# Optimization experiments

Hardware: AMD Instinct MI355X
Metric: run time of the kernel (lower is better)

The kernel has to match this reference:

```python
import jax, jax.numpy as jnp
import numpy as np

B, N, D, H = 32, 2048, 65, 64  # batch, seq_len, in_dim+out_dim, hid
GAMMA = 0.0001


def setup_inputs() -> dict:
    key = jax.random.key(0)
    kx, kq, kk, kv = jax.random.split(key, 4)
    x = jax.random.normal(kx, (B, N, D), dtype=jnp.float32)
    std_qk = (GAMMA / D) ** 0.5
    Wq = jax.random.normal(kq, (H, D), dtype=jnp.float32) * std_qk
    Wk = jax.random.normal(kk, (H, D), dtype=jnp.float32) * std_qk
    Wv = jax.random.normal(kv, (D, D), dtype=jnp.float32) * GAMMA
    return {"x": x, "Wq": Wq, "Wk": Wk, "Wv": Wv}


def reference(x, Wq, Wk, Wv):
    # Linear projections (torch nn.Linear: x @ W^T)
    Q = jnp.einsum('bnd,hd->bnh', x, Wq)  # [B, N, H]
    K = jnp.einsum('bnd,hd->bnh', x, Wk)  # [B, N, H]
    V = jnp.einsum('bnd,ed->bne', x, Wv)  # [B, N, D]
    # Non-softmax linear attention: (Q K^T) V, as written in the module
    scores = jnp.einsum('bnh,bmh->bnm', Q, K)  # [B, N, N]
    out = jnp.einsum('bnm,bmd->bnd', scores, V)  # [B, N, D]
    return out
```

## Files before the change

### kernel.cpp

```cpp
#include <hip/hip_runtime.h>

#define BB 32
#define NN 2048
#define DD 65
#define HH 64
#define ST 68
#define TILE (DD * ST)
#define CC 32

__device__ __forceinline__ float4 f4add(float4 a, float4 b) {
  return make_float4(a.x + b.x, a.y + b.y, a.z + b.z, a.w + b.w);
}

#define GL2LDS(g, l)                                             \
  __builtin_amdgcn_global_load_lds(                              \
      (const __attribute__((address_space(1))) void*)(g),        \
      (__attribute__((address_space(3))) void*)(l), 16, 0, 0)

__global__ __launch_bounds__(256, 6) void k1_gram(const float* __restrict__ x,
                                                  float* __restrict__ P) {
  __shared__ __align__(16) float Xl[64 * ST];
  const int t = (int)threadIdx.x;
  const int tx = t & 15, ty = t >> 4;
  const int blk = (int)blockIdx.x;
  const int b = blk >> 5, c = blk & 31;
  const float* src = x + ((size_t)b * NN + (size_t)c * 64) * DD;

  {
#pragma unroll
    for (int p = 0; p < 3; p++) {
      float tmp[6];
      const int cnt = (p == 2) ? 5 : 6;
#pragma unroll
      for (int q = 0; q < 6; q++) {
        const int idx = t + 256 * (6 * p + q);
        if (q < cnt && idx < 64 * DD) tmp[q] = src[idx];
      }
#pragma unroll
      for (int q = 0; q < 6; q++) {
        const int idx = t + 256 * (6 * p + q);
        if (q < cnt && idx < 64 * DD) {
          const int r = idx / DD;
          Xl[r * ST + (idx - r * DD)] = tmp[q];
        }
      }
    }
  }
  __syncthreads();

  float g[4][4] = {};
  float g64[4] = {};
  float gcc = 0.f;
  for (int n = 0; n < 64; n++) {
    float rowf[4], colf[4];
    *(float4*)rowf = *(const float4*)&Xl[n * ST + 4 * ty];
    *(float4*)colf = *(const float4*)&Xl[n * ST + 4 * tx];
    const float x64 = Xl[n * ST + 64];
#pragma unroll
    for (int r = 0; r < 4; r++)
#pragma unroll
      for (int cc = 0; cc < 4; cc++)
        g[r][cc] = fmaf(rowf[r], colf[cc], g[r][cc]);
#pragma unroll
    for (int cc = 0; cc < 4; cc++) g64[cc] = fmaf(x64, colf[cc], g64[cc]);
    gcc = fmaf(x64, x64, gcc);
  }
  float* Pp = P + (size_t)blk * TILE;
#pragma unroll
  for (int r = 0; r < 4; r++)
    *(float4*)&Pp[(4 * ty + r) * ST + 4 * tx] = *(float4*)g[r];
  if (ty == 0) {
    *(float4*)&Pp[64 * ST + 4 * tx] = *(float4*)g64;
#pragma unroll
    for (int cc = 0; cc < 4; cc++)
      Pp[(4 * tx + cc) * ST + 64] = g64[cc];
    if (tx == 0) Pp[64 * ST + 64] = gcc;
  }
}

__global__ __launch_bounds__(256) void kred(const float* __restrict__ P,
                                            float* __restrict__ G) {
  const int t = (int)threadIdx.x;
  const int blk = (int)blockIdx.x;
  const int b = blk / 5, s = blk - b * 5;
  const int Q = TILE / 4;
  const int i4 = s * 256 + t;
  if (i4 < Q) {
    const float4* Pb = (const float4*)(P + (size_t)b * CC * TILE);
    float4 acc = make_float4(0.f, 0.f, 0.f, 0.f);
#pragma unroll
    for (int grp = 0; grp < 4; grp++) {
      float4 v[8];
#pragma unroll
      for (int cc = 0; cc < 8; cc++)
        v[cc] = Pb[(size_t)(8 * grp + cc) * Q + i4];
#pragma unroll
      for (int stp = 4; stp >= 1; stp >>= 1)
#pragma unroll
        for (int cc = 0; cc < stp; cc++) v[cc] = f4add(v[cc], v[cc + stp]);
      acc = f4add(acc, v[0]);
    }
    ((float4*)(G + (size_t)b * TILE))[i4] = acc;
  }
}

__global__ __launch_bounds__(256) void k2_chain(
    const float* __restrict__ Wq, const float* __restrict__ Wk,
    const float* __restrict__ Wv, const float* __restrict__ G,
    float* __restrict__ Tm) {
  __shared__ __align__(16) float WqL[HH * ST];
  __shared__ __align__(16) float WkL[HH * ST];
  __shared__ __align__(16) float GL[TILE];
  __shared__ __align__(16) float WvT[TILE];
  __shared__ __align__(16) float Mr[8 * ST];
  __shared__ __align__(16) float Rr[8 * ST];

  const int t = (int)threadIdx.x;
  const int tx = t & 31, ty = t >> 5;
  const int blk = (int)blockIdx.x;
  const int b = blk / 9, rg = blk - b * 9;
  const int i = 8 * rg + ty;
  const bool alive = (i < DD);
  const int ic = alive ? i : 0;

  {
    float tq[17], tk[17];
#pragma unroll
    for (int q = 0; q < 17; q++) {
      const int idx = t + 256 * q;
      if (idx < HH * DD) { tq[q] = Wq[idx]; tk[q] = Wk[idx]; }
    }
#pragma unroll
    for (int q = 0; q < 17; q++) {
      const int idx = t + 256 * q;
      if (idx < HH * DD) {
        const int r = idx / DD, cc = idx - r * DD;
        WqL[r * ST + cc] = tq[q];
        WkL[r * ST + cc] = tk[q];
      }
    }
  }
  {
    const float4* Gb4 = (const float4*)(G + (size_t)b * TILE);
    float4 tG[5];
#pragma unroll
    for (int q = 0; q < 5; q++) {
      const int i4 = t + 256 * q;
      if (i4 < TILE / 4) tG[q] = Gb4[i4];
    }
#pragma unroll
    for (int q = 0; q < 5; q++) {
      const int i4 = t + 256 * q;
      if (i4 < TILE / 4) *((float4*)GL + i4) = tG[q];
    }
  }
  {
    float tv[17];
#pragma unroll
    for (int q = 0; q < 17; q++) {
      const int idx = t + 256 * q;
      if (idx < DD * DD) tv[q] = Wv[idx];
    }
#pragma unroll
    for (int q = 0; q < 17; q++) {
      const int idx = t + 256 * q;
      if (idx < DD * DD) {
        const int j = idx / DD, k = idx - j * DD;
        WvT[k * ST + j] = tv[q];
      }
    }
  }
  __syncthreads();

  {
    float m0 = 0.f, m1 = 0.f, m2 = 0.f;
    for (int h = 0; h < HH; h++) {
      const float wq = WqL[h * ST + ic];
      m0 = fmaf(wq, WkL[h * ST + tx], m0);
      m1 = fmaf(wq, WkL[h * ST + tx + 32], m1);
      m2 = fmaf(wq, WkL[h * ST + 64], m2);
    }
    if (alive) {
      Mr[ty * ST + tx] = m0;
      Mr[ty * ST + tx + 32] = m1;
      if (tx == 0) Mr[ty * ST + 64] = m2;
    }
  }
  __syncthreads();

  {
    float r0 = 0.f, r1 = 0.f, r2 = 0.f;
    for (int k = 0; k < DD; k++) {
      const float mm = Mr[ty * ST + k];
      r0 = fmaf(mm, GL[k * ST + tx], r0);
      r1 = fmaf(mm, GL[k * ST + tx + 32], r1);
      r2 = fmaf(mm, GL[k * ST + 64], r2);
    }
    if (alive) {
      Rr[ty * ST + tx] = r0;
      Rr[ty * ST + tx + 32] = r1;
      if (tx == 0) Rr[ty * ST + 64] = r2;
    }
  }
  __syncthreads();

  {
    float t0 = 0.f, t1 = 0.f, t2 = 0.f;
    for (int k = 0; k < DD; k++) {
      const float rv = Rr[ty * ST + k];
      t0 = fmaf(rv, WvT[k * ST + tx], t0);
      t1 = fmaf(rv, WvT[k * ST + tx + 32], t1);
      t2 = fmaf(rv, WvT[k * ST + 64], t2);
    }
    if (alive) {
      float* Tb = Tm + (size_t)b * TILE + (size_t)i * ST;
      Tb[tx] = t0;
      Tb[tx + 32] = t1;
      if (tx == 0) Tb[64] = t2;
    }
  }
}

__global__ __launch_bounds__(256, 4) void k3_out(const float* __restrict__ x,
                                                 const float* __restrict__ Tt,
                                                 float* __restrict__ out) {
  __shared__ __align__(16) float Tl[TILE];
  __shared__ __align__(16) float Xl[64 * ST];
  const int t = (int)threadIdx.x;
  const int tx = t & 15, ty = t >> 4;
  const int wid = t >> 6, lane = t & 63;
  const int blk = (int)blockIdx.x;
  const int b = blk >> 5;
  const int rb = (blk & 31) * 64;
  const float4* Tg4 = (const float4*)(Tt + (size_t)b * TILE);
  const float* src = x + ((size_t)b * NN + rb) * DD;

#pragma unroll
  for (int q = 0; q < 4; q++) {
    const int s = q * 256 + wid * 64 + lane;
    GL2LDS(Tg4 + s, Tl + (size_t)(q * 256 + wid * 64) * 4);
  }
  {
    const int s = 1024 + wid * 64 + lane;
    if (s < TILE / 4) GL2LDS(Tg4 + s, Tl + (size_t)(1024 + wid * 64) * 4);
  }

#pragma unroll
  for (int p = 0; p < 2; p++) {
    float tmp[9];
    const int cnt = (p == 1) ? 8 : 9;
#pragma unroll
    for (int q = 0; q < 9; q++) {
      const int idx = t + 256 * (9 * p + q);
      if (q < cnt && idx < 64 * DD) tmp[q] = src[idx];
    }
#pragma unroll
    for (int q = 0; q < 9; q++) {
      const int idx = t + 256 * (9 * p + q);
      if (q < cnt && idx < 64 * DD) {
        const int r = idx / DD;
        Xl[r * ST + (idx - r * DD)] = tmp[q];
      }
    }
  }
  __syncthreads();

  float o[4][4] = {}, o64[4] = {};
  for (int kk = 0; kk < 64; kk += 4) {
    float xa4[4][4];
    float tb4[4][4];
    float t64e[4];
#pragma unroll
    for (int r = 0; r < 4; r++)
      *(float4*)xa4[r] = *(const float4*)&Xl[(4 * ty + r) * ST + kk];
#pragma unroll
    for (int e = 0; e < 4; e++)
      *(float4*)tb4[e] = *(const float4*)&Tl[(kk + e) * ST + 4 * tx];
#pragma unroll
    for (int e = 0; e < 4; e++) t64e[e] = Tl[(kk + e) * ST + 64];
#pragma unroll
    for (int e = 0; e < 4; e++) {
#pragma unroll
      for (int r = 0; r < 4; r++)
#pragma unroll
        for (int cc = 0; cc < 4; cc++)
          o[r][cc] = fmaf(xa4[r][e], tb4[e][cc], o[r][cc]);
#pragma unroll
      for (int r = 0; r < 4; r++)
        o64[r] = fmaf(xa4[r][e], t64e[e], o64[r]);
    }
  }
  {
    float xs[4];
#pragma unroll
    for (int r = 0; r < 4; r++) xs[r] = Xl[(4 * ty + r) * ST + 64];
    float tb[4];
    *(float4*)tb = *(const float4*)&Tl[64 * ST + 4 * tx];
    const float t64 = Tl[64 * ST + 64];
#pragma unroll
    for (int r = 0; r < 4; r++) {
#pragma unroll
      for (int cc = 0; cc < 4; cc++)
        o[r][cc] = fmaf(xs[r], tb[cc], o[r][cc]);
      o64[r] = fmaf(xs[r], t64, o64[r]);
    }
  }

  __syncthreads();
  float* Ol = Xl;
#pragma unroll
  for (int r = 0; r < 4; r++) {
#pragma unroll
    for (int cc = 0; cc < 4; cc++)
      Ol[(4 * ty + r) * DD + 4 * tx + cc] = o[r][cc];
  }
  if (tx == 0) {
#pragma unroll
    for (int r = 0; r < 4; r++) Ol[(4 * ty + r) * DD + 64] = o64[r];
  }
  __syncthreads();
  {
    float4* ob4 = (float4*)(out + ((size_t)b * NN + rb) * DD);
    const float4* Ol4 = (const float4*)Ol;
#pragma unroll
    for (int q = 0; q < 5; q++) {
      const int i4 = t + 256 * q;
      if (i4 < (64 * DD) / 4) ob4[i4] = Ol4[i4];
    }
  }
}

extern "C" void kernel_launch(void* const* d_in, const int* in_sizes, int n_in,
                              void* d_out, int out_size, void* d_ws,
                              size_t ws_size, hipStream_t stream) {
  const float* x = (const float*)d_in[0];
  const float* Wq = (const float*)d_in[1];
  const float* Wk = (const float*)d_in[2];
  const float* Wv = (const float*)d_in[3];
  float* out = (float*)d_out;

  float* P = (float*)d_ws;
  float* G = P + (size_t)BB * CC * TILE;
  float* Tm = G + (size_t)BB * TILE;

  k1_gram<<<BB * CC, 256, 0, stream>>>(x, P);
  kred<<<BB * 5, 256, 0, stream>>>(P, G);
  k2_chain<<<BB * 9, 256, 0, stream>>>(Wq, Wk, Wv, G, Tm);
  k3_out<<<BB * CC, 256, 0, stream>>>(x, Tm, out);
  (void)in_sizes; (void)n_in; (void)out_size; (void)ws_size;
}
```

Baseline: 117.1 us.

## Map one 64-row chunk per wavefront with 8x8 register tiles in gram and output kernels

```diff
diff --git a/kernel.cpp b/kernel.cpp
--- a/kernel.cpp
+++ b/kernel.cpp
@@ -17,64 +17,75 @@
       (const __attribute__((address_space(1))) void*)(g),        \
       (__attribute__((address_space(3))) void*)(l), 16, 0, 0)
 
-__global__ __launch_bounds__(256, 6) void k1_gram(const float* __restrict__ x,
+__global__ __launch_bounds__(128, 2) void k1_gram(const float* __restrict__ x,
                                                   float* __restrict__ P) {
-  __shared__ __align__(16) float Xl[64 * ST];
+  __shared__ __align__(16) float Xl[2][64 * ST];
   const int t = (int)threadIdx.x;
-  const int tx = t & 15, ty = t >> 4;
-  const int blk = (int)blockIdx.x;
-  const int b = blk >> 5, c = blk & 31;
-  const float* src = x + ((size_t)b * NN + (size_t)c * 64) * DD;
-
-  {
-#pragma unroll
-    for (int p = 0; p < 3; p++) {
-      float tmp[6];
-      const int cnt = (p == 2) ? 5 : 6;
-#pragma unroll
-      for (int q = 0; q < 6; q++) {
-        const int idx = t + 256 * (6 * p + q);
-        if (q < cnt && idx < 64 * DD) tmp[q] = src[idx];
-      }
-#pragma unroll
-      for (int q = 0; q < 6; q++) {
-        const int idx = t + 256 * (6 * p + q);
-        if (q < cnt && idx < 64 * DD) {
-          const int r = idx / DD;
-          Xl[r * ST + (idx - r * DD)] = tmp[q];
+  const int w = t >> 6, lane = t & 63;
+  const int tx8 = lane & 7, ty8 = lane >> 3;
+  const int chunk = (int)blockIdx.x * 2 + w;
+  const int b = chunk >> 5, c = chunk & 31;
+  const float4* src4 =
+      (const float4*)(x + ((size_t)b * NN + (size_t)c * 64) * DD);
+  float* Xw = Xl[w];
+
+#pragma unroll
+  for (int p = 0; p < 2; p++) {
+    float4 tmp[9];
+    const int cnt = p ? 8 : 9;
+#pragma unroll
+    for (int q = 0; q < 9; q++) {
+      const int i4 = lane + 64 * (9 * p + q);
+      if (q < cnt && i4 < 1040) tmp[q] = src4[i4];
+    }
+#pragma unroll
+    for (int q = 0; q < 9; q++) {
+      const int i4 = lane + 64 * (9 * p + q);
+      if (q < cnt && i4 < 1040) {
+        const int f = 4 * i4;
+        const float vv[4] = {tmp[q].x, tmp[q].y, tmp[q].z, tmp[q].w};
+#pragma unroll
+        for (int j = 0; j < 4; j++) {
+          const int r = (f + j) / DD, cc = (f + j) - r * DD;
+          Xw[r * ST + cc] = vv[j];
         }
       }
     }
   }
-  __syncthreads();
-
-  float g[4][4] = {};
-  float g64[4] = {};
+
+  float g[8][8] = {};
+  float f64[8] = {};
   float gcc = 0.f;
   for (int n = 0; n < 64; n++) {
-    float rowf[4], colf[4];
-    *(float4*)rowf = *(const float4*)&Xl[n * ST + 4 * ty];
-    *(float4*)colf = *(const float4*)&Xl[n * ST + 4 * tx];
-    const float x64 = Xl[n * ST + 64];
-#pragma unroll
-    for (int r = 0; r < 4; r++)
-#pragma unroll
-      for (int cc = 0; cc < 4; cc++)
+    float rowf[8], colf[8];
+    *(float4*)&rowf[0] = *(const float4*)&Xw[n * ST + 8 * ty8];
+    *(float4*)&rowf[4] = *(const float4*)&Xw[n * ST + 8 * ty8 + 4];
+    *(float4*)&colf[0] = *(const float4*)&Xw[n * ST + 8 * tx8];
+    *(float4*)&colf[4] = *(const float4*)&Xw[n * ST + 8 * tx8 + 4];
+    const float x64 = Xw[n * ST + 64];
+#pragma unroll
+    for (int r = 0; r < 8; r++)
+#pragma unroll
+      for (int cc = 0; cc < 8; cc++)
         g[r][cc] = fmaf(rowf[r], colf[cc], g[r][cc]);
 #pragma unroll
-    for (int cc = 0; cc < 4; cc++) g64[cc] = fmaf(x64, colf[cc], g64[cc]);
+    for (int cc = 0; cc < 8; cc++) f64[cc] = fmaf(x64, colf[cc], f64[cc]);
     gcc = fmaf(x64, x64, gcc);
   }
-  float* Pp = P + (size_t)blk * TILE;
-#pragma unroll
-  for (int r = 0; r < 4; r++)
-    *(float4*)&Pp[(4 * ty + r) * ST + 4 * tx] = *(float4*)g[r];
-  if (ty == 0) {
-    *(float4*)&Pp[64 * ST + 4 * tx] = *(float4*)g64;
-#pragma unroll
-    for (int cc = 0; cc < 4; cc++)
-      Pp[(4 * tx + cc) * ST + 64] = g64[cc];
-    if (tx == 0) Pp[64 * ST + 64] = gcc;
+
+  float* Pp = P + (size_t)chunk * TILE;
+#pragma unroll
+  for (int r = 0; r < 8; r++) {
+    *(float4*)&Pp[(8 * ty8 + r) * ST + 8 * tx8] = *(float4*)&g[r][0];
+    *(float4*)&Pp[(8 * ty8 + r) * ST + 8 * tx8 + 4] = *(float4*)&g[r][4];
+  }
+  if (ty8 == 0) {
+#pragma unroll
+    for (int cc = 0; cc < 8; cc++) {
+      Pp[64 * ST + 8 * tx8 + cc] = f64[cc];
+      Pp[(8 * tx8 + cc) * ST + 64] = f64[cc];
+    }
+    if (tx8 == 0) Pp[64 * ST + 64] = gcc;
   }
 }
 
@@ -221,112 +232,105 @@
   }
 }
 
-__global__ __launch_bounds__(256, 4) void k3_out(const float* __restrict__ x,
+__global__ __launch_bounds__(128, 2) void k3_out(const float* __restrict__ x,
                                                  const float* __restrict__ Tt,
                                                  float* __restrict__ out) {
   __shared__ __align__(16) float Tl[TILE];
-  __shared__ __align__(16) float Xl[64 * ST];
+  __shared__ __align__(16) float Xl[2][64 * ST];
   const int t = (int)threadIdx.x;
-  const int tx = t & 15, ty = t >> 4;
-  const int wid = t >> 6, lane = t & 63;
+  const int w = t >> 6, lane = t & 63;
+  const int tx8 = lane & 7, ty8 = lane >> 3;
   const int blk = (int)blockIdx.x;
-  const int b = blk >> 5;
-  const int rb = (blk & 31) * 64;
+  const int b = blk >> 4;
+  const int chunk = (blk & 15) * 2 + w;
   const float4* Tg4 = (const float4*)(Tt + (size_t)b * TILE);
-  const float* src = x + ((size_t)b * NN + rb) * DD;
-
-#pragma unroll
-  for (int q = 0; q < 4; q++) {
-    const int s = q * 256 + wid * 64 + lane;
-    GL2LDS(Tg4 + s, Tl + (size_t)(q * 256 + wid * 64) * 4);
-  }
-  {
-    const int s = 1024 + wid * 64 + lane;
-    if (s < TILE / 4) GL2LDS(Tg4 + s, Tl + (size_t)(1024 + wid * 64) * 4);
+  const float4* src4 =
+      (const float4*)(x + ((size_t)b * NN + (size_t)chunk * 64) * DD);
+  float* Xw = Xl[w];
+
+#pragma unroll
+  for (int q = 0; q < 8; q++)
+    GL2LDS(Tg4 + q * 128 + w * 64 + lane,
+           Tl + (size_t)(q * 128 + w * 64) * 4);
+  {
+    const int s = 1024 + w * 64 + lane;
+    if (s < TILE / 4) GL2LDS(Tg4 + s, Tl + (size_t)(1024 + w * 64) * 4);
   }
 
 #pragma unroll
   for (int p = 0; p < 2; p++) {
-    float tmp[9];
-    const int cnt = (p == 1) ? 8 : 9;
+    float4 tmp[9];
+    const int cnt = p ? 8 : 9;
 #pragma unroll
     for (int q = 0; q < 9; q++) {
-      const int idx = t + 256 * (9 * p + q);
-      if (q < cnt && idx < 64 * DD) tmp[q] = src[idx];
+      const int i4 = lane + 64 * (9 * p + q);
+      if (q < cnt && i4 < 1040) tmp[q] = src4[i4];
     }
 #pragma unroll
     for (int q = 0; q < 9; q++) {
-      const int idx = t + 256 * (9 * p + q);
-      if (q < cnt && idx < 64 * DD) {
-        const int r = idx / DD;
-        Xl[r * ST + (idx - r * DD)] = tmp[q];
+      const int i4 = lane + 64 * (9 * p + q);
+      if (q < cnt && i4 < 1040) {
+        const int f = 4 * i4;
+        const float vv[4] = {tmp[q].x, tmp[q].y, tmp[q].z, tmp[q].w};
+#pragma unroll
+        for (int j = 0; j < 4; j++) {
+          const int r = (f + j) / DD, cc = (f + j) - r * DD;
+          Xw[r * ST + cc] = vv[j];
+        }
       }
     }
   }
   __syncthreads();
 
-  float o[4][4] = {}, o64[4] = {};
+  float o[8][8] = {}, o64[8] = {};
   for (int kk = 0; kk < 64; kk += 4) {
-    float xa4[4][4];
-    float tb4[4][4];
-    float t64e[4];
-#pragma unroll
-    for (int r = 0; r < 4; r++)
-      *(float4*)xa4[r] = *(const float4*)&Xl[(4 * ty + r) * ST + kk];
-#pragma unroll
-    for (int e = 0; e < 4; e++)
-      *(float4*)tb4[e] = *(const float4*)&Tl[(kk + e) * ST + 4 * tx];
-#pragma unroll
-    for (int e = 0; e < 4; e++) t64e[e] = Tl[(kk + e) * ST + 64];
+    float xa[8][4];
+#pragma unroll
+    for (int r = 0; r < 8; r++)
+      *(float4*)xa[r] = *(const float4*)&Xw[(8 * ty8 + r) * ST + kk];
 #pragma unroll
     for (int e = 0; e < 4; e++) {
-#pragma unroll
-      for (int r = 0; r < 4; r++)
-#pragma unroll
-        for (int cc = 0; cc < 4; cc++)
-          o[r][cc] = fmaf(xa4[r][e], tb4[e][cc], o[r][cc]);
-#pragma unroll
-      for (int r = 0; r < 4; r++)
-        o64[r] = fmaf(xa4[r][e], t64e[e], o64[r]);
-    }
-  }
-  {
-    float xs[4];
-#pragma unroll
-    for (int r = 0; r < 4; r++) xs[r] = Xl[(4 * ty + r) * ST + 64];
-    float tb[4];
-    *(float4*)tb = *(const float4*)&Tl[64 * ST + 4 * tx];
+      float tb[8];
+      *(float4*)&tb[0] = *(const float4*)&Tl[(kk + e) * ST + 8 * tx8];
+      *(float4*)&tb[4] = *(const float4*)&Tl[(kk + e) * ST + 8 * tx8 + 4];
+      const float t64 = Tl[(kk + e) * ST + 64];
+#pragma unroll
+      for (int r = 0; r < 8; r++) {
+#pragma unroll
+        for (int cc = 0; cc < 8; cc++)
+          o[r][cc] = fmaf(xa[r][e], tb[cc], o[r][cc]);
+        o64[r] = fmaf(xa[r][e], t64, o64[r]);
+      }
+    }
+  }
+  {
+    float tb[8];
+    *(float4*)&tb[0] = *(const float4*)&Tl[64 * ST + 8 * tx8];
+    *(float4*)&tb[4] = *(const float4*)&Tl[64 * ST + 8 * tx8 + 4];
     const float t64 = Tl[64 * ST + 64];
 #pragma unroll
-    for (int r = 0; r < 4; r++) {
-#pragma unroll
-      for (int cc = 0; cc < 4; cc++)
-        o[r][cc] = fmaf(xs[r], tb[cc], o[r][cc]);
-      o64[r] = fmaf(xs[r], t64, o64[r]);
-    }
-  }
-
-  __syncthreads();
-  float* Ol = Xl;
-#pragma unroll
-  for (int r = 0; r < 4; r++) {
-#pragma unroll
-    for (int cc = 0; cc < 4; cc++)
-      Ol[(4 * ty + r) * DD + 4 * tx + cc] = o[r][cc];
-  }
-  if (tx == 0) {
-#pragma unroll
-    for (int r = 0; r < 4; r++) Ol[(4 * ty + r) * DD + 64] = o64[r];
-  }
-  __syncthreads();
-  {
-    float4* ob4 = (float4*)(out + ((size_t)b * NN + rb) * DD);
-    const float4* Ol4 = (const float4*)Ol;
-#pragma unroll
-    for (int q = 0; q < 5; q++) {
-      const int i4 = t + 256 * q;
-      if (i4 < (64 * DD) / 4) ob4[i4] = Ol4[i4];
-    }
+    for (int r = 0; r < 8; r++) {
+      const float xs = Xw[(8 * ty8 + r) * ST + 64];
+#pragma unroll
+      for (int cc = 0; cc < 8; cc++)
+        o[r][cc] = fmaf(xs, tb[cc], o[r][cc]);
+      o64[r] = fmaf(xs, t64, o64[r]);
+    }
+  }
+
+  float* Ow = Xw;
+#pragma unroll
+  for (int r = 0; r < 8; r++) {
+#pragma unroll
+    for (int cc = 0; cc < 8; cc++)
+      Ow[(8 * ty8 + r) * DD + 8 * tx8 + cc] = o[r][cc];
+    if (tx8 == 0) Ow[(8 * ty8 + r) * DD + 64] = o64[r];
+  }
+  float4* ob4 = (float4*)(out + ((size_t)b * NN + (size_t)chunk * 64) * DD);
+#pragma unroll
+  for (int q = 0; q < 17; q++) {
+    const int i4 = lane + 64 * q;
+    if (i4 < 1040) ob4[i4] = ((const float4*)Ow)[i4];
   }
 }
 
@@ -343,9 +347,9 @@
   float* G = P + (size_t)BB * CC * TILE;
   float* Tm = G + (size_t)BB * TILE;
 
-  k1_gram<<<BB * CC, 256, 0, stream>>>(x, P);
+  k1_gram<<<BB * CC / 2, 128, 0, stream>>>(x, P);
   kred<<<BB * 5, 256, 0, stream>>>(P, G);
   k2_chain<<<BB * 9, 256, 0, stream>>>(Wq, Wk, Wv, G, Tm);
-  k3_out<<<BB * CC, 256, 0, stream>>>(x, Tm, out);
+  k3_out<<<BB * CC / 2, 128, 0, stream>>>(x, Tm, out);
   (void)in_sizes; (void)n_in; (void)out_size; (void)ws_size;
 }
```

Result: slower. 127.8 us (+9.1%).
